# Kernel tuning notes

Hardware: AMD Instinct MI355X
Metric: run time of the kernel (lower is better)

## Reference

```python
import jax, jax.numpy as jnp
import numpy as np

THETA = 5.0
NUM_CLASSES = 8
MAX_ITERS = 15


def _maxpool3(x):
    # x: [N, H, W]; 3x3 max pool, stride 1, SAME padding (matches F.max_pool2d k=3,s=1,p=1)
    return jax.lax.reduce_window(x, -jnp.inf, jax.lax.max,
                                 (1, 3, 3), (1, 1, 1), 'SAME')


def setup_inputs() -> dict:
    key = jax.random.key(0)
    k1, k2 = jax.random.split(key)
    inputs = jax.random.normal(k1, (16, NUM_CLASSES, 512, 512), dtype=jnp.float32)
    targets = jax.random.randint(k2, (16, 512, 512), 0, NUM_CLASSES)
    return {"inputs": inputs, "targets": targets}


def _boundaries(targets):
    # One-hot per class, morphological gradient (dilate - erode) > 0, summed over classes.
    B, H, W = targets.shape
    oh = jax.nn.one_hot(targets, NUM_CLASSES, dtype=jnp.float32)  # [B,H,W,C]
    x = oh.transpose(0, 3, 1, 2).reshape(B * NUM_CLASSES, H, W)   # [B*C,H,W]
    dilated = _maxpool3(x)
    eroded = -_maxpool3(-x)
    grad = (dilated - eroded).reshape(B, NUM_CLASSES, H, W).sum(axis=1)
    return (grad > 0).astype(jnp.float32)  # [B,H,W]


def _distance_map(boundary):
    # Iterative dilation distance transform, capped at MAX_ITERS (unreached pixels stay 0,
    # matching the original module's quirk).
    def body(i, carry):
        dist, cur = carry
        dil = _maxpool3(cur)
        new_pix = (dil > cur).astype(jnp.float32)
        return (dist + new_pix * (i + 1), dil)

    dist0 = jnp.zeros_like(boundary)
    dist, _ = jax.lax.fori_loop(0, MAX_ITERS, body, (dist0, boundary))
    return dist


def reference(inputs, targets):
    boundary = _boundaries(targets)            # [B,H,W]
    dist = _distance_map(boundary)             # [B,H,W]
    weights = jnp.exp(-dist / THETA)
    logp = jax.nn.log_softmax(inputs, axis=1)  # [B,C,H,W]
    ce = -jnp.take_along_axis(logp, targets[:, None, :, :], axis=1)[:, 0]  # [B,H,W]
    return jnp.mean(weights * ce)
```

## Files before the change

### kernel.cpp

```cpp
#include <hip/hip_runtime.h>
#include <stdint.h>

#define IMG_H 512
#define IMG_W 512
#define NB 16
#define NC 8
#define HW (IMG_H * IMG_W)

#define TILE 64
#define HALO 15
#define CROWS 94
#define TROWS 96
#define TCOLS 96
#define TSTRIDE 100
#define NTASK (CROWS * 3)
#define NBLK (NB * 64)

typedef float f4 __attribute__((ext_vector_type(4)));

__global__ __launch_bounds__(256) void distce_kernel(const float* __restrict__ in,
                                                     const int* __restrict__ tgt,
                                                     float* __restrict__ partials) {
    __shared__ uint8_t  tg[TROWS][TSTRIDE];
    __shared__ uint32_t cur[2][CROWS][5];
    __shared__ uint8_t  dtile[TILE][TILE];
    int b   = blockIdx.x >> 6;
    int tid = blockIdx.x & 63;
    int ty = tid >> 3, tx = tid & 7;
    int ry = ty * TILE, rx = tx * TILE;
    int t = threadIdx.x;
    const int* tgtb = tgt + (size_t)b * HW;

    ((uint4*)dtile)[t] = make_uint4(0u, 0u, 0u, 0u);

    if (tx >= 1 && tx <= 6) {
        #pragma unroll
        for (int k = 0; k < 9; k++) {
            int tau = t + 256 * k;
            int r = tau / 24, c4 = tau % 24;
            int gy = min(max(ry - 16 + r, 0), IMG_H - 1);
            const int4* rowp = (const int4*)(tgtb + (size_t)gy * IMG_W + rx - 16);
            int4 v = rowp[c4];
            ((uint32_t*)&tg[r][0])[c4] =
                (uint32_t)(v.x & 255) | ((uint32_t)(v.y & 255) << 8) |
                ((uint32_t)(v.z & 255) << 16) | ((uint32_t)(v.w & 255) << 24);
        }
    } else {
        #pragma unroll
        for (int k = 0; k < 36; k++) {
            int tau = t + 256 * k;
            int r = tau / TCOLS, c = tau % TCOLS;
            int gy = min(max(ry - 16 + r, 0), IMG_H - 1);
            int gx = min(max(rx - 16 + c, 0), IMG_W - 1);
            tg[r][c] = (uint8_t)tgtb[gy * IMG_W + gx];
        }
    }
    __syncthreads();

    auto bword = [&](int r, int w) -> uint32_t {
        int rr = r + 1;
        int gy = ry - 15 + r;
        uint32_t word = 0u;
        if (gy >= 0 && gy < IMG_H) {
            uint32_t Wc[10], Wa[10], Wb[10];
            const uint32_t* pc = (const uint32_t*)&tg[rr][0];
            const uint32_t* pa = (const uint32_t*)&tg[rr - 1][0];
            const uint32_t* pb = (const uint32_t*)&tg[rr + 1][0];
            #pragma unroll
            for (int k = 0; k < 10; k++) {
                int idx = 8 * w - 1 + k;
                idx = min(max(idx, 0), 23);
                Wc[k] = pc[idx]; Wa[k] = pa[idx]; Wb[k] = pb[idx];
            }
            #pragma unroll
            for (int i = 0; i < 8; i++) {
                uint32_t T = Wc[i + 1];
                uint32_t L = (Wc[i + 1] << 8) | (Wc[i] >> 24);
                uint32_t R = (Wc[i + 1] >> 8) | (Wc[i + 2] << 24);
                uint32_t a = (T ^ L) | (T ^ R);
                uint32_t C2 = Wa[i + 1];
                uint32_t L2 = (Wa[i + 1] << 8) | (Wa[i] >> 24);
                uint32_t R2 = (Wa[i + 1] >> 8) | (Wa[i + 2] << 24);
                a |= (T ^ C2) | (T ^ L2) | (T ^ R2);
                uint32_t C3 = Wb[i + 1];
                uint32_t L3 = (Wb[i + 1] << 8) | (Wb[i] >> 24);
                uint32_t R3 = (Wb[i + 1] >> 8) | (Wb[i + 2] << 24);
                a |= (T ^ C3) | (T ^ L3) | (T ^ R3);
                uint32_t t1  = (a & 0x7F7F7F7Fu) + 0x7F7F7F7Fu;
                uint32_t nzb = ((t1 | a) & 0x80808080u) >> 7;
                word |= (((nzb * 0x01020408u) >> 24) & 0xFu) << (4 * i);
            }
            if (tx == 0 && w == 0) word &= 0xFFFF0000u;
            if (tx == 7 && w == 2) word &= 0x0000FFFFu;
        }
        return word;
    };
    int r0 = t / 3, w0 = t % 3;
    uint32_t o0 = bword(r0, w0);
    cur[0][r0][w0] = o0;
    bool has1 = (t + 256) < NTASK;
    int r1 = (t + 256) / 3, w1 = (t + 256) % 3;
    if (has1) cur[0][r1][w1] = bword(r1, w1);
    uint32_t lm0 = (w0 == 0) ? 0xFFFF0000u : (w0 == 1) ? 0xFFFFFFFFu : 0x0000FFFFu;
    bool inner0 = (r0 >= HALO && r0 < HALO + TILE);

    int cnt = __syncthreads_count(inner0 && ((o0 | ~lm0) != 0xFFFFFFFFu));
    if (cnt != 0) {
        for (int it = 1; it <= 15; ++it) {
            int pr = (it + 1) & 1, pw = it & 1;
            uint32_t n0 = 0u;
            #pragma unroll
            for (int dr = -1; dr <= 1; dr++) {
                int rr = r0 + dr;
                if ((unsigned)rr >= (unsigned)CROWS) continue;
                uint32_t vv = cur[pr][rr][w0];
                uint32_t lf = (w0 > 0) ? cur[pr][rr][w0 - 1] : 0u;
                uint32_t rg = (w0 < 2) ? cur[pr][rr][w0 + 1] : 0u;
                n0 |= vv | (vv << 1) | (vv >> 1) | (lf >> 31) | (rg << 31);
            }
            cur[pw][r0][w0] = n0;
            uint32_t nb = (n0 & ~o0) & lm0;
            o0 = n0;
            if (inner0) {
                uint32_t x = nb;
                while (x) { int bit = __ffs(x) - 1; x &= x - 1;
                            dtile[r0 - HALO][w0 * 32 + bit - 16] = (uint8_t)it; }
            }
            if (has1) {
                uint32_t n1 = 0u;
                #pragma unroll
                for (int dr = -1; dr <= 1; dr++) {
                    int rr = r1 + dr;
                    if ((unsigned)rr >= (unsigned)CROWS) continue;
                    uint32_t vv = cur[pr][rr][w1];
                    uint32_t lf = (w1 > 0) ? cur[pr][rr][w1 - 1] : 0u;
                    uint32_t rg = (w1 < 2) ? cur[pr][rr][w1 + 1] : 0u;
                    n1 |= vv | (vv << 1) | (vv >> 1) | (lf >> 31) | (rg << 31);
                }
                cur[pw][r1][w1] = n1;
            }
            cnt = __syncthreads_count(inner0 && ((n0 | ~lm0) != 0xFFFFFFFFu));
            if (cnt == 0) break;
        }
    }

    float partial = 0.0f;
    const float* inb = in + (size_t)b * NC * HW;
    #pragma unroll
    for (int g = 0; g < 4; g++) {
        int q = t + 256 * g;
        int row = q >> 4, quad = q & 15;
        const float* base = inb + (size_t)(ry + row) * IMG_W + rx + quad * 4;
        float v[NC][4];
        #pragma unroll
        for (int c = 0; c < NC; c++) {
            f4 f = *(const f4*)(base + (size_t)c * HW);
            v[c][0] = f.x; v[c][1] = f.y; v[c][2] = f.z; v[c][3] = f.w;
        }
        uint32_t tw = ((const uint32_t*)&tg[16 + row][0])[4 + quad];
        uint32_t d4 = *(const uint32_t*)&dtile[row][quad * 4];
        #pragma unroll
        for (int j = 0; j < 4; j++) {
            float mx = v[0][j];
            #pragma unroll
            for (int c = 1; c < NC; c++) mx = fmaxf(mx, v[c][j]);
            float s = 0.0f;
            #pragma unroll
            for (int c = 0; c < NC; c++) s += __expf(v[c][j] - mx);
            float lse = mx + __logf(s);
            int tc = (int)((tw >> (8 * j)) & 0xFFu);
            float lt = v[0][j];
            #pragma unroll
            for (int c = 1; c < NC; c++) lt = (tc == c) ? v[c][j] : lt;
            float ce = lse - lt;
            float d = (float)((d4 >> (8 * j)) & 0xFFu);
            partial += __expf(d * -0.2f) * ce;
        }
    }
    #pragma unroll
    for (int off = 32; off > 0; off >>= 1) partial += __shfl_down(partial, off);
    __shared__ float wsums[4];
    int lane = t & 63;
    int wid = t >> 6;
    if (lane == 0) wsums[wid] = partial;
    __syncthreads();
    if (t == 0)
        partials[blockIdx.x] = wsums[0] + wsums[1] + wsums[2] + wsums[3];
}

__global__ __launch_bounds__(256) void reduce_kernel(const float* __restrict__ partials,
                                                     float* __restrict__ out) {
    double s = 0.0;
    #pragma unroll
    for (int i = 0; i < NBLK / 256; i++)
        s += (double)partials[threadIdx.x + 256 * i];
    #pragma unroll
    for (int off = 32; off > 0; off >>= 1) s += __shfl_down(s, off);
    __shared__ double wsums[4];
    int lane = threadIdx.x & 63;
    int wid = threadIdx.x >> 6;
    if (lane == 0) wsums[wid] = s;
    __syncthreads();
    if (threadIdx.x == 0) {
        double tot = wsums[0] + wsums[1] + wsums[2] + wsums[3];
        out[0] = (float)(tot * (1.0 / (double)((size_t)NB * HW)));
    }
}

extern "C" void kernel_launch(void* const* d_in, const int* in_sizes, int n_in,
                              void* d_out, int out_size, void* d_ws, size_t ws_size,
                              hipStream_t stream) {
    const float* in  = (const float*)d_in[0];
    const int*   tgt = (const int*)d_in[1];
    float* out = (float*)d_out;

    float* partials = (float*)((char*)d_ws + 256);

    distce_kernel<<<NBLK, 256, 0, stream>>>(in, tgt, partials);
    reduce_kernel<<<1, 256, 0, stream>>>(partials, out);
}
```

Measured before the change: 32.07 us.

## Halve tile height to 32x64 and double block count with one task per thread

Tiles shrink from 64x64 to 32x64, which doubles the grid to 2048 blocks. The bit-packed distance-transform rows now fit in 186 tasks, so each thread handles at most one row-word instead of two, and the second-task code path is removed. Launch bounds ask for 8 blocks per CU to raise occupancy. In exchange the 15-row halo is a larger share of each tile, so more redundant target loads and dilation work are done per output pixel.

```diff
diff --git a/kernel.cpp b/kernel.cpp
--- a/kernel.cpp
+++ b/kernel.cpp
@@ -7,35 +7,36 @@
 #define NC 8
 #define HW (IMG_H * IMG_W)
 
-#define TILE 64
+#define TH 32
+#define TW 64
 #define HALO 15
-#define CROWS 94
-#define TROWS 96
+#define CROWS (TH + 2 * HALO)
+#define TROWS (TH + 32)
 #define TCOLS 96
 #define TSTRIDE 100
 #define NTASK (CROWS * 3)
-#define NBLK (NB * 64)
+#define NBLK (NB * 128)
 
 typedef float f4 __attribute__((ext_vector_type(4)));
 
-__global__ __launch_bounds__(256) void distce_kernel(const float* __restrict__ in,
-                                                     const int* __restrict__ tgt,
-                                                     float* __restrict__ partials) {
+__global__ __launch_bounds__(256, 8) void distce_kernel(const float* __restrict__ in,
+                                                        const int* __restrict__ tgt,
+                                                        float* __restrict__ partials) {
     __shared__ uint8_t  tg[TROWS][TSTRIDE];
     __shared__ uint32_t cur[2][CROWS][5];
-    __shared__ uint8_t  dtile[TILE][TILE];
-    int b   = blockIdx.x >> 6;
-    int tid = blockIdx.x & 63;
+    __shared__ uint8_t  dtile[TH][TW];
+    int b   = blockIdx.x >> 7;
+    int tid = blockIdx.x & 127;
     int ty = tid >> 3, tx = tid & 7;
-    int ry = ty * TILE, rx = tx * TILE;
+    int ry = ty * TH, rx = tx * TW;
     int t = threadIdx.x;
     const int* tgtb = tgt + (size_t)b * HW;
 
-    ((uint4*)dtile)[t] = make_uint4(0u, 0u, 0u, 0u);
+    if (t < 128) ((uint4*)dtile)[t] = make_uint4(0u, 0u, 0u, 0u);
 
     if (tx >= 1 && tx <= 6) {
         #pragma unroll
-        for (int k = 0; k < 9; k++) {
+        for (int k = 0; k < 6; k++) {
             int tau = t + 256 * k;
             int r = tau / 24, c4 = tau % 24;
             int gy = min(max(ry - 16 + r, 0), IMG_H - 1);
@@ -47,7 +48,7 @@
         }
     } else {
         #pragma unroll
-        for (int k = 0; k < 36; k++) {
+        for (int k = 0; k < 24; k++) {
             int tau = t + 256 * k;
             int r = tau / TCOLS, c = tau % TCOLS;
             int gy = min(max(ry - 16 + r, 0), IMG_H - 1);
@@ -57,10 +58,12 @@
     }
     __syncthreads();
 
-    auto bword = [&](int r, int w) -> uint32_t {
-        int rr = r + 1;
-        int gy = ry - 15 + r;
-        uint32_t word = 0u;
+    bool has0 = t < NTASK;
+    int r0 = has0 ? (t / 3) : 0, w0 = has0 ? (t % 3) : 0;
+    uint32_t o0 = 0u;
+    if (has0) {
+        int rr = r0 + 1;
+        int gy = ry - 15 + r0;
         if (gy >= 0 && gy < IMG_H) {
             uint32_t Wc[10], Wa[10], Wb[10];
             const uint32_t* pc = (const uint32_t*)&tg[rr][0];
@@ -68,7 +71,7 @@
             const uint32_t* pb = (const uint32_t*)&tg[rr + 1][0];
             #pragma unroll
             for (int k = 0; k < 10; k++) {
-                int idx = 8 * w - 1 + k;
+                int idx = 8 * w0 - 1 + k;
                 idx = min(max(idx, 0), 23);
                 Wc[k] = pc[idx]; Wa[k] = pa[idx]; Wb[k] = pb[idx];
             }
@@ -88,56 +91,39 @@
                 a |= (T ^ C3) | (T ^ L3) | (T ^ R3);
                 uint32_t t1  = (a & 0x7F7F7F7Fu) + 0x7F7F7F7Fu;
                 uint32_t nzb = ((t1 | a) & 0x80808080u) >> 7;
-                word |= (((nzb * 0x01020408u) >> 24) & 0xFu) << (4 * i);
+                o0 |= (((nzb * 0x01020408u) >> 24) & 0xFu) << (4 * i);
             }
-            if (tx == 0 && w == 0) word &= 0xFFFF0000u;
-            if (tx == 7 && w == 2) word &= 0x0000FFFFu;
-        }
-        return word;
-    };
-    int r0 = t / 3, w0 = t % 3;
-    uint32_t o0 = bword(r0, w0);
-    cur[0][r0][w0] = o0;
-    bool has1 = (t + 256) < NTASK;
-    int r1 = (t + 256) / 3, w1 = (t + 256) % 3;
-    if (has1) cur[0][r1][w1] = bword(r1, w1);
+            if (tx == 0 && w0 == 0) o0 &= 0xFFFF0000u;
+            if (tx == 7 && w0 == 2) o0 &= 0x0000FFFFu;
+        }
+        cur[0][r0][w0] = o0;
+    }
     uint32_t lm0 = (w0 == 0) ? 0xFFFF0000u : (w0 == 1) ? 0xFFFFFFFFu : 0x0000FFFFu;
-    bool inner0 = (r0 >= HALO && r0 < HALO + TILE);
+    bool inner0 = has0 && (r0 >= HALO && r0 < HALO + TH);
 
     int cnt = __syncthreads_count(inner0 && ((o0 | ~lm0) != 0xFFFFFFFFu));
     if (cnt != 0) {
         for (int it = 1; it <= 15; ++it) {
             int pr = (it + 1) & 1, pw = it & 1;
             uint32_t n0 = 0u;
-            #pragma unroll
-            for (int dr = -1; dr <= 1; dr++) {
-                int rr = r0 + dr;
-                if ((unsigned)rr >= (unsigned)CROWS) continue;
-                uint32_t vv = cur[pr][rr][w0];
-                uint32_t lf = (w0 > 0) ? cur[pr][rr][w0 - 1] : 0u;
-                uint32_t rg = (w0 < 2) ? cur[pr][rr][w0 + 1] : 0u;
-                n0 |= vv | (vv << 1) | (vv >> 1) | (lf >> 31) | (rg << 31);
-            }
-            cur[pw][r0][w0] = n0;
-            uint32_t nb = (n0 & ~o0) & lm0;
-            o0 = n0;
-            if (inner0) {
-                uint32_t x = nb;
-                while (x) { int bit = __ffs(x) - 1; x &= x - 1;
-                            dtile[r0 - HALO][w0 * 32 + bit - 16] = (uint8_t)it; }
-            }
-            if (has1) {
-                uint32_t n1 = 0u;
+            if (has0) {
                 #pragma unroll
                 for (int dr = -1; dr <= 1; dr++) {
-                    int rr = r1 + dr;
+                    int rr = r0 + dr;
                     if ((unsigned)rr >= (unsigned)CROWS) continue;
-                    uint32_t vv = cur[pr][rr][w1];
-                    uint32_t lf = (w1 > 0) ? cur[pr][rr][w1 - 1] : 0u;
-                    uint32_t rg = (w1 < 2) ? cur[pr][rr][w1 + 1] : 0u;
-                    n1 |= vv | (vv << 1) | (vv >> 1) | (lf >> 31) | (rg << 31);
+                    uint32_t vv = cur[pr][rr][w0];
+                    uint32_t lf = (w0 > 0) ? cur[pr][rr][w0 - 1] : 0u;
+                    uint32_t rg = (w0 < 2) ? cur[pr][rr][w0 + 1] : 0u;
+                    n0 |= vv | (vv << 1) | (vv >> 1) | (lf >> 31) | (rg << 31);
                 }
-                cur[pw][r1][w1] = n1;
+                cur[pw][r0][w0] = n0;
+                uint32_t nb = (n0 & ~o0) & lm0;
+                o0 = n0;
+                if (inner0) {
+                    uint32_t x = nb;
+                    while (x) { int bit = __ffs(x) - 1; x &= x - 1;
+                                dtile[r0 - HALO][w0 * 32 + bit - 16] = (uint8_t)it; }
+                }
             }
             cnt = __syncthreads_count(inner0 && ((n0 | ~lm0) != 0xFFFFFFFFu));
             if (cnt == 0) break;
@@ -147,7 +133,7 @@
     float partial = 0.0f;
     const float* inb = in + (size_t)b * NC * HW;
     #pragma unroll
-    for (int g = 0; g < 4; g++) {
+    for (int g = 0; g < 2; g++) {
         int q = t + 256 * g;
         int row = q >> 4, quad = q & 15;
         const float* base = inb + (size_t)(ry + row) * IMG_W + rx + quad * 4;
```

Result: slower. 33.87 us (+5.6%).
